# Kernel tuning notes

Measured on AMD Instinct MI355X. Metric: run time of the kernel, lower is better.

Reference implementation:

```python
import jax, jax.numpy as jnp
import numpy as np

D_K = 512  # module-level global used for the scale factor


def setup_inputs() -> dict:
    key = jax.random.key(0)
    kq, kk, kv, km = jax.random.split(key, 4)
    B, H, L = 4, 8, 1024
    Q = jax.random.normal(kq, (B, H, L, D_K), dtype=jnp.float32)
    K = jax.random.normal(kk, (B, H, L, D_K), dtype=jnp.float32)
    V = jax.random.normal(kv, (B, H, L, D_K), dtype=jnp.float32)
    attn_mask = jax.random.randint(km, (B, H, L, L), 0, 2).astype(jnp.bool_)
    return {"Q": Q, "K": K, "V": V, "attn_mask": attn_mask}


def reference(Q, K, V, attn_mask):
    scale = 1.0 / np.sqrt(D_K).astype(np.float32)
    # [B,H,Lq,Lk]
    scores = jnp.einsum('bhqd,bhkd->bhqk', Q, K) * scale
    scores = jnp.where(attn_mask, jnp.float32(-1e9), scores)
    attn = jax.nn.softmax(scores, axis=-1)
    context = jnp.einsum('bhqk,bhkd->bhqd', attn, V)
    return (context, attn)
```

## Files before the change

### kernel.cpp

```cpp
#include <hip/hip_runtime.h>
#include <hip/hip_bf16.h>

constexpr int BH  = 32;
constexpr int LQ  = 1024;
constexpr int DK  = 512;
constexpr float SCALE = 0.04419417382415922f;

using short8 = __attribute__((ext_vector_type(8))) short;
using f32x4  = __attribute__((ext_vector_type(4))) float;

__device__ __forceinline__ unsigned short cvt_bf16(float x) {
  unsigned int u = __builtin_bit_cast(unsigned int, x);
  u += 0x7FFFu + ((u >> 16) & 1u);
  return (unsigned short)(u >> 16);
}
__device__ __forceinline__ float bf2f(unsigned short s) {
  return __builtin_bit_cast(float, (unsigned int)s << 16);
}
__device__ __forceinline__ unsigned int pack2(float a, float b) {
  return (unsigned int)cvt_bf16(a) | ((unsigned int)cvt_bf16(b) << 16);
}

__device__ __forceinline__ void lds_load16(const void* g, void* l) {
  __builtin_amdgcn_global_load_lds(
      (const __attribute__((address_space(1))) unsigned int*)g,
      (__attribute__((address_space(3))) unsigned int*)l, 16, 0, 0);
}

__global__ __launch_bounds__(256) void cvt_f32_bf16(
    const float* __restrict__ src, unsigned short* __restrict__ dst, int n8) {
  int i = blockIdx.x * 256 + threadIdx.x;
  const int stride = gridDim.x * 256;
  for (; i < n8; i += stride) {
    float4 a = ((const float4*)src)[(size_t)i * 2];
    float4 b = ((const float4*)src)[(size_t)i * 2 + 1];
    unsigned short us[8] __attribute__((aligned(16)));
    us[0]=cvt_bf16(a.x); us[1]=cvt_bf16(a.y); us[2]=cvt_bf16(a.z); us[3]=cvt_bf16(a.w);
    us[4]=cvt_bf16(b.x); us[5]=cvt_bf16(b.y); us[6]=cvt_bf16(b.z); us[7]=cvt_bf16(b.w);
    ((short8*)dst)[i] = *(short8*)us;
  }
}

__global__ __launch_bounds__(256) void qk_exp_kernel(
    const unsigned short* __restrict__ A, const unsigned short* __restrict__ B,
    const int* __restrict__ mask, unsigned short* __restrict__ P,
    float* __restrict__ partials) {
  __shared__ __attribute__((aligned(16))) unsigned short smem[16384];
  unsigned short* As = smem;
  unsigned short* Bs = smem + 8192;

  int flat = blockIdx.x + 8 * (blockIdx.y + 8 * blockIdx.z);
  flat = (flat % 8) * 256 + flat / 8;
  const int bx = flat % 8;
  const int by = (flat / 8) % 8;
  const int bh = flat / 64;

  const int t = threadIdx.x;
  const int lane = t & 63, wave = t >> 6;
  const int wr = wave >> 1, wc = wave & 1;
  const int fr = lane & 15, fq = lane >> 4;
  const int m0 = by * 128, n0 = bx * 128;

  const char* Ab = (const char*)A + ((size_t)bh * LQ + m0) * 1024;
  const char* Bb = (const char*)B + ((size_t)bh * LQ + n0) * 1024;

  unsigned int orv = 0;
  {
    const unsigned int* mw = (const unsigned int*)mask;
    #pragma unroll
    for (int i = 0; i < 64; ++i) orv |= mw[i];
  }
  const bool byteMode = (orv > 1u);

  f32x4 acc[4][4];
  #pragma unroll
  for (int i = 0; i < 4; ++i)
    #pragma unroll
    for (int j = 0; j < 4; ++j) acc[i][j] = (f32x4){0.f, 0.f, 0.f, 0.f};

  for (int kb = 0; kb < DK * 2; kb += 128) {
    __syncthreads();
    #pragma unroll
    for (int i = 0; i < 4; ++i) {
      const int p  = i * 4096 + t * 16;
      const int r  = p >> 7;
      const int ch = (p >> 4) & 7;
      const int sw = ((ch ^ (r & 7)) << 4);
      lds_load16(Ab + (size_t)r * 1024 + kb + sw, (char*)As + wave * 1024 + i * 4096);
      lds_load16(Bb + (size_t)r * 1024 + kb + sw, (char*)Bs + wave * 1024 + i * 4096);
    }
    __syncthreads();

    #pragma unroll
    for (int kk = 0; kk < 2; ++kk) {
      short8 a[4], b[4];
      #pragma unroll
      for (int mi = 0; mi < 4; ++mi) {
        const int r  = wr * 64 + mi * 16 + fr;
        const int ch = (kk * 4 + fq) ^ (r & 7);
        a[mi] = *(const short8*)((const char*)As + r * 128 + ch * 16);
      }
      #pragma unroll
      for (int ni = 0; ni < 4; ++ni) {
        const int r  = wc * 64 + ni * 16 + fr;
        const int ch = (kk * 4 + fq) ^ (r & 7);
        b[ni] = *(const short8*)((const char*)Bs + r * 128 + ch * 16);
      }
      #pragma unroll
      for (int mi = 0; mi < 4; ++mi)
        #pragma unroll
        for (int ni = 0; ni < 4; ++ni)
          acc[mi][ni] = __builtin_amdgcn_mfma_f32_16x16x32_bf16(a[mi], b[ni], acc[mi][ni], 0, 0, 0);
    }
  }

  __syncthreads();
  unsigned short* Cs = smem;
  #pragma unroll
  for (int mi = 0; mi < 4; ++mi)
    #pragma unroll
    for (int ni = 0; ni < 4; ++ni) {
      const int col = wc * 64 + ni * 16 + fr;
      #pragma unroll
      for (int r = 0; r < 4; ++r) {
        const int row = wr * 64 + mi * 16 + fq * 4 + r;
        Cs[row * 128 + col] = cvt_bf16(__expf(acc[mi][ni][r] * SCALE));
      }
    }
  __syncthreads();

  const int rl = t >> 4;
  const int cl = (t & 15) * 8;
  const size_t pbase = (size_t)bh * LQ * LQ;
  #pragma unroll
  for (int rb = 0; rb < 8; ++rb) {
    const int rloc = rb * 16 + rl;
    const int rg   = m0 + rloc;
    const size_t gidx = pbase + (size_t)rg * LQ + (n0 + cl);
    short8 sv = *(const short8*)&Cs[rloc * 128 + cl];
    bool mk[8];
    if (byteMode) {
      const unsigned char* mb = (const unsigned char*)mask + gidx;
      uint2 w = *(const uint2*)mb;
      #pragma unroll
      for (int j = 0; j < 4; ++j) mk[j]     = ((w.x >> (8 * j)) & 255u) != 0u;
      #pragma unroll
      for (int j = 0; j < 4; ++j) mk[4 + j] = ((w.y >> (8 * j)) & 255u) != 0u;
    } else {
      int4 w0 = *(const int4*)(mask + gidx);
      int4 w1 = *(const int4*)(mask + gidx + 4);
      mk[0] = w0.x != 0; mk[1] = w0.y != 0; mk[2] = w0.z != 0; mk[3] = w0.w != 0;
      mk[4] = w1.x != 0; mk[5] = w1.y != 0; mk[6] = w1.z != 0; mk[7] = w1.w != 0;
    }
    unsigned short out[8] __attribute__((aligned(16)));
    float s = 0.f;
    #pragma unroll
    for (int j = 0; j < 8; ++j) {
      unsigned short v = mk[j] ? (unsigned short)0 : (unsigned short)sv[j];
      out[j] = v;
      s += bf2f(v);
    }
    *(short8*)(P + gidx) = *(short8*)out;
    s += __shfl_xor(s, 1); s += __shfl_xor(s, 2);
    s += __shfl_xor(s, 4); s += __shfl_xor(s, 8);
    if ((t & 15) == 0)
      partials[((size_t)bh * LQ + rg) * 8 + bx] = s;
  }
}

__global__ __launch_bounds__(256) void attn_fin(
    const unsigned short* __restrict__ P, const float* __restrict__ partials,
    float* __restrict__ attn) {
  const int ch = blockIdx.x, rb64 = blockIdx.y, bh = blockIdx.z;
  const int m0 = rb64 * 64;
  __shared__ float invs[64];
  const int t = threadIdx.x;
  if (t < 64) {
    const float* pp = partials + ((size_t)bh * LQ + m0 + t) * 8;
    float s = ((pp[0] + pp[1]) + (pp[2] + pp[3])) + ((pp[4] + pp[5]) + (pp[6] + pp[7]));
    invs[t] = 1.0f / s;
  }
  __syncthreads();
  const size_t pbase = (size_t)bh * LQ * LQ;
  const int c0 = ch * 512;
  #pragma unroll
  for (int rb = 0; rb < 4; ++rb) {
    const int rloc = rb * 16 + (t >> 4);
    const int row  = m0 + rloc;
    const float inv = invs[rloc];
    const size_t base = pbase + (size_t)row * LQ + c0 + (t & 15) * 8;
    #pragma unroll
    for (int j = 0; j < 4; ++j) {
      short8 sv = *(const short8*)(P + base + j * 128);
      float4 o0, o1;
      o0.x = bf2f((unsigned short)sv[0]) * inv;
      o0.y = bf2f((unsigned short)sv[1]) * inv;
      o0.z = bf2f((unsigned short)sv[2]) * inv;
      o0.w = bf2f((unsigned short)sv[3]) * inv;
      o1.x = bf2f((unsigned short)sv[4]) * inv;
      o1.y = bf2f((unsigned short)sv[5]) * inv;
      o1.z = bf2f((unsigned short)sv[6]) * inv;
      o1.w = bf2f((unsigned short)sv[7]) * inv;
      *(float4*)(attn + base + j * 128)     = o0;
      *(float4*)(attn + base + j * 128 + 4) = o1;
    }
  }
}

__global__ __launch_bounds__(256) void pv2_kernel(
    const unsigned short* __restrict__ P, const float* __restrict__ V,
    const float* __restrict__ partials, float* __restrict__ O) {
  __shared__ __attribute__((aligned(16))) unsigned short As[8192];
  __shared__ __attribute__((aligned(16))) unsigned short BsV[128 * 72];
  __shared__ float invsL[128];

  int flat = blockIdx.x + 4 * (blockIdx.y + 8 * blockIdx.z);
  flat = (flat % 8) * 128 + flat / 8;
  const int bx = flat % 4;
  const int by = (flat / 4) % 8;
  const int bh = flat / 32;

  const int t = threadIdx.x;
  const int lane = t & 63, wave = t >> 6;
  const int wr = wave >> 1, wc = wave & 1;
  const int fr = lane & 15, fq = lane >> 4;
  const int m0 = by * 128, n0 = bx * 128;

  if (t < 128) {
    const float* pp = partials + ((size_t)bh * LQ + m0 + t) * 8;
    float s = ((pp[0] + pp[1]) + (pp[2] + pp[3])) + ((pp[4] + pp[5]) + (pp[6] + pp[7]));
    invsL[t] = 1.0f / s;
  }

  const char* Ab  = (const char*)P + ((size_t)bh * LQ + m0) * 2048;
  const float* Vb = V + (size_t)bh * LQ * DK + n0;

  f32x4 acc[4][4];
  #pragma unroll
  for (int i = 0; i < 4; ++i)
    #pragma unroll
    for (int j = 0; j < 4; ++j) acc[i][j] = (f32x4){0.f, 0.f, 0.f, 0.f};

  const int g  = t >> 5;
  const int nl = t & 31;

  for (int k0 = 0; k0 < LQ; k0 += 64) {
    __syncthreads();
    #pragma unroll
    for (int i = 0; i < 4; ++i) {
      const int p  = i * 4096 + t * 16;
      const int r  = p >> 7;
      const int ch = (p >> 4) & 7;
      const int sw = ((ch ^ (r & 7)) << 4);
      lds_load16(Ab + (size_t)r * 2048 + k0 * 2 + sw, (char*)As + wave * 1024 + i * 4096);
    }
    float vf[8][4];
    #pragma unroll
    for (int i = 0; i < 8; ++i) {
      const size_t rb = (size_t)(k0 + 8 * g + i) * DK;
      #pragma unroll
      for (int jn = 0; jn < 4; ++jn)
        vf[i][jn] = Vb[rb + nl + 32 * jn];
    }
    #pragma unroll
    for (int jn = 0; jn < 4; ++jn) {
      const int n = nl + 32 * jn;
      uint2 w0, w1;
      w0.x = pack2(vf[0][jn], vf[1][jn]); w0.y = pack2(vf[2][jn], vf[3][jn]);
      w1.x = pack2(vf[4][jn], vf[5][jn]); w1.y = pack2(vf[6][jn], vf[7][jn]);
      *(uint2*)((char*)BsV + n * 144 + 16 * g)     = w0;
      *(uint2*)((char*)BsV + n * 144 + 16 * g + 8) = w1;
    }
    __syncthreads();

    #pragma unroll
    for (int kk = 0; kk < 2; ++kk) {
      short8 a[4], b[4];
      #pragma unroll
      for (int mi = 0; mi < 4; ++mi) {
        const int r  = wr * 64 + mi * 16 + fr;
        const int ch = (kk * 4 + fq) ^ (r & 7);
        a[mi] = *(const short8*)((const char*)As + r * 128 + ch * 16);
      }
      #pragma unroll
      for (int ni = 0; ni < 4; ++ni) {
        const int r = wc * 64 + ni * 16 + fr;
        b[ni] = *(const short8*)((const char*)BsV + r * 144 + (kk * 4 + fq) * 16);
      }
      #pragma unroll
      for (int mi = 0; mi < 4; ++mi)
        #pragma unroll
        for (int ni = 0; ni < 4; ++ni)
          acc[mi][ni] = __builtin_amdgcn_mfma_f32_16x16x32_bf16(a[mi], b[ni], acc[mi][ni], 0, 0, 0);
    }
  }

  const size_t obase = (size_t)bh * LQ * DK;
  #pragma unroll
  for (int mi = 0; mi < 4; ++mi)
    #pragma unroll
    for (int ni = 0; ni < 4; ++ni) {
      const int col = n0 + wc * 64 + ni * 16 + fr;
      #pragma unroll
      for (int r = 0; r < 4; ++r) {
        const int rloc = wr * 64 + mi * 16 + fq * 4 + r;
        O[obase + (size_t)(m0 + rloc) * DK + col] = acc[mi][ni][r] * invsL[rloc];
      }
    }
}

__global__ __launch_bounds__(256) void qk_mask_kernel(
    const float* __restrict__ Q, const float* __restrict__ Kmat,
    const int* __restrict__ mask, float* __restrict__ S) {
  __shared__ __attribute__((aligned(16))) unsigned short Asf[128][40];
  __shared__ __attribute__((aligned(16))) unsigned short Bsf[128][40];
  const int t = threadIdx.x;
  const int lane = t & 63, wave = t >> 6;
  const int wr = wave >> 1, wc = wave & 1;
  const int fr = lane & 15, fq = lane >> 4;
  const int bh = blockIdx.z;
  const int m0 = blockIdx.y * 128, n0 = blockIdx.x * 128;
  const float* Qb = Q + (size_t)bh * LQ * DK;
  const float* Kb = Kmat + (size_t)bh * LQ * DK;
  unsigned int orv = 0;
  { const unsigned int* mw = (const unsigned int*)mask;
    #pragma unroll
    for (int i = 0; i < 64; ++i) orv |= mw[i]; }
  const bool byteMode = (orv > 1u);
  f32x4 acc[4][4];
  #pragma unroll
  for (int i = 0; i < 4; ++i)
    #pragma unroll
    for (int j = 0; j < 4; ++j) acc[i][j] = (f32x4){0.f,0.f,0.f,0.f};
  const int sr = t >> 1, sc = (t & 1) * 16;
  for (int kd = 0; kd < DK; kd += 32) {
    __syncthreads();
    { const float4* qa = (const float4*)(Qb + (size_t)(m0+sr)*DK + kd + sc);
      float fv[16];
      #pragma unroll
      for (int i = 0; i < 4; ++i) { float4 x = qa[i];
        fv[4*i]=x.x; fv[4*i+1]=x.y; fv[4*i+2]=x.z; fv[4*i+3]=x.w; }
      unsigned short us[16] __attribute__((aligned(16)));
      #pragma unroll
      for (int i = 0; i < 16; ++i) us[i] = cvt_bf16(fv[i]);
      *(short8*)&Asf[sr][sc]   = *(short8*)&us[0];
      *(short8*)&Asf[sr][sc+8] = *(short8*)&us[8]; }
    { const float4* ka = (const float4*)(Kb + (size_t)(n0+sr)*DK + kd + sc);
      float fv[16];
      #pragma unroll
      for (int i = 0; i < 4; ++i) { float4 x = ka[i];
        fv[4*i]=x.x; fv[4*i+1]=x.y; fv[4*i+2]=x.z; fv[4*i+3]=x.w; }
      unsigned short us[16] __attribute__((aligned(16)));
      #pragma unroll
      for (int i = 0; i < 16; ++i) us[i] = cvt_bf16(fv[i]);
      *(short8*)&Bsf[sr][sc]   = *(short8*)&us[0];
      *(short8*)&Bsf[sr][sc+8] = *(short8*)&us[8]; }
    __syncthreads();
    short8 a[4], b[4];
    #pragma unroll
    for (int mi = 0; mi < 4; ++mi) a[mi] = *(const short8*)&Asf[wr*64+mi*16+fr][fq*8];
    #pragma unroll
    for (int ni = 0; ni < 4; ++ni) b[ni] = *(const short8*)&Bsf[wc*64+ni*16+fr][fq*8];
    #pragma unroll
    for (int mi = 0; mi < 4; ++mi)
      #pragma unroll
      for (int ni = 0; ni < 4; ++ni)
        acc[mi][ni] = __builtin_amdgcn_mfma_f32_16x16x32_bf16(a[mi], b[ni], acc[mi][ni], 0, 0, 0);
  }
  const size_t sbase = (size_t)bh * LQ * LQ;
  const unsigned char* mb = (const unsigned char*)mask;
  #pragma unroll
  for (int mi = 0; mi < 4; ++mi)
    #pragma unroll
    for (int ni = 0; ni < 4; ++ni) {
      const int col = n0 + wc*64 + ni*16 + fr;
      #pragma unroll
      for (int r = 0; r < 4; ++r) {
        const int row = m0 + wr*64 + mi*16 + fq*4 + r;
        const size_t idx = sbase + (size_t)row * LQ + col;
        float s = acc[mi][ni][r] * SCALE;
        const bool msk = byteMode ? (mb[idx] != 0) : (mask[idx] != 0);
        S[idx] = msk ? -1e9f : s;
      }
    }
}

__global__ __launch_bounds__(256) void softmax_kernel(float* __restrict__ A) {
  const int row = blockIdx.x;
  float4* rp = (float4*)(A + (size_t)row * LQ);
  const int t = threadIdx.x;
  float4 v = rp[t];
  float m = fmaxf(fmaxf(v.x, v.y), fmaxf(v.z, v.w));
  #pragma unroll
  for (int off = 32; off >= 1; off >>= 1) m = fmaxf(m, __shfl_xor(m, off, 64));
  __shared__ float redm[4];
  const int wv = t >> 6, ln = t & 63;
  if (ln == 0) redm[wv] = m;
  __syncthreads();
  m = fmaxf(fmaxf(redm[0], redm[1]), fmaxf(redm[2], redm[3]));
  float4 e;
  e.x = expf(v.x - m); e.y = expf(v.y - m); e.z = expf(v.z - m); e.w = expf(v.w - m);
  float s = (e.x + e.y) + (e.z + e.w);
  #pragma unroll
  for (int off = 32; off >= 1; off >>= 1) s += __shfl_xor(s, off, 64);
  __shared__ float reds2[4];
  if (ln == 0) reds2[wv] = s;
  __syncthreads();
  s = (reds2[0] + reds2[1]) + (reds2[2] + reds2[3]);
  const float inv = 1.0f / s;
  e.x *= inv; e.y *= inv; e.z *= inv; e.w *= inv;
  rp[t] = e;
}

__global__ __launch_bounds__(256) void pv_kernel(
    const float* __restrict__ P, const float* __restrict__ V, float* __restrict__ O) {
  __shared__ __attribute__((aligned(16))) unsigned short Ps[128][40];
  __shared__ __attribute__((aligned(16))) unsigned short Vtl[128][40];
  const int t = threadIdx.x;
  const int lane = t & 63, wave = t >> 6;
  const int wr = wave >> 1, wc = wave & 1;
  const int fr = lane & 15, fq = lane >> 4;
  const int bh = blockIdx.z;
  const int m0 = blockIdx.y * 128, n0 = blockIdx.x * 128;
  const float* Pb = P + (size_t)bh * LQ * LQ;
  const float* Vb = V + (size_t)bh * LQ * DK;
  f32x4 acc[4][4];
  #pragma unroll
  for (int i = 0; i < 4; ++i)
    #pragma unroll
    for (int j = 0; j < 4; ++j) acc[i][j] = (f32x4){0.f,0.f,0.f,0.f};
  const int sr = t >> 1, sc = (t & 1) * 16;
  const int kk = (t & 15) * 2, nn = (t >> 4) * 8;
  for (int k0 = 0; k0 < LQ; k0 += 32) {
    __syncthreads();
    { const float4* pa = (const float4*)(Pb + (size_t)(m0+sr)*LQ + k0 + sc);
      float fv[16];
      #pragma unroll
      for (int i = 0; i < 4; ++i) { float4 x = pa[i];
        fv[4*i]=x.x; fv[4*i+1]=x.y; fv[4*i+2]=x.z; fv[4*i+3]=x.w; }
      unsigned short us[16] __attribute__((aligned(16)));
      #pragma unroll
      for (int i = 0; i < 16; ++i) us[i] = cvt_bf16(fv[i]);
      *(short8*)&Ps[sr][sc]   = *(short8*)&us[0];
      *(short8*)&Ps[sr][sc+8] = *(short8*)&us[8]; }
    { const float* v0p = Vb + (size_t)(k0+kk)*DK + n0 + nn;
      const float* v1p = v0p + DK;
      float4 a0 = *(const float4*)v0p, a1 = *(const float4*)(v0p+4);
      float4 b0 = *(const float4*)v1p, b1 = *(const float4*)(v1p+4);
      float r0[8] = {a0.x,a0.y,a0.z,a0.w,a1.x,a1.y,a1.z,a1.w};
      float r1[8] = {b0.x,b0.y,b0.z,b0.w,b1.x,b1.y,b1.z,b1.w};
      #pragma unroll
      for (int i = 0; i < 8; ++i) {
        unsigned int pk = (unsigned int)cvt_bf16(r0[i]) | ((unsigned int)cvt_bf16(r1[i]) << 16);
        *(unsigned int*)&Vtl[nn+i][kk] = pk; } }
    __syncthreads();
    short8 a[4], b[4];
    #pragma unroll
    for (int mi = 0; mi < 4; ++mi) a[mi] = *(const short8*)&Ps[wr*64+mi*16+fr][fq*8];
    #pragma unroll
    for (int ni = 0; ni < 4; ++ni) b[ni] = *(const short8*)&Vtl[wc*64+ni*16+fr][fq*8];
    #pragma unroll
    for (int mi = 0; mi < 4; ++mi)
      #pragma unroll
      for (int ni = 0; ni < 4; ++ni)
        acc[mi][ni] = __builtin_amdgcn_mfma_f32_16x16x32_bf16(a[mi], b[ni], acc[mi][ni], 0, 0, 0);
  }
  const size_t obase = (size_t)bh * LQ * DK;
  #pragma unroll
  for (int mi = 0; mi < 4; ++mi)
    #pragma unroll
    for (int ni = 0; ni < 4; ++ni) {
      const int col = n0 + wc*64 + ni*16 + fr;
      #pragma unroll
      for (int r = 0; r < 4; ++r) {
        const int row = m0 + wr*64 + mi*16 + fq*4 + r;
        O[obase + (size_t)row * DK + col] = acc[mi][ni][r];
      }
    }
}

extern "C" void kernel_launch(void* const* d_in, const int* in_sizes, int n_in,
                              void* d_out, int out_size, void* d_ws, size_t ws_size,
                              hipStream_t stream) {
  const float* Q    = (const float*)d_in[0];
  const float* K    = (const float*)d_in[1];
  const float* V    = (const float*)d_in[2];
  const int*   mask = (const int*)d_in[3];

  float* ctx  = (float*)d_out;
  float* attn = ctx + (size_t)BH * LQ * DK;

  const size_t NE = (size_t)BH * LQ * DK;
  const size_t P_BYTES  = (size_t)BH * LQ * LQ * 2;
  const size_t WS_NEED  = P_BYTES + (size_t)BH * LQ * 8 * 4;

  if (ws_size >= WS_NEED) {
    unsigned short* Pp       = (unsigned short*)d_ws;
    float*          partials = (float*)((char*)d_ws + P_BYTES);
    unsigned short* Qb = (unsigned short*)ctx;
    unsigned short* Kb = Qb + NE;

    cvt_f32_bf16<<<dim3(2048), 256, 0, stream>>>(Q, Qb, (int)(NE / 8));
    cvt_f32_bf16<<<dim3(2048), 256, 0, stream>>>(K, Kb, (int)(NE / 8));
    qk_exp_kernel<<<dim3(8, 8, BH), 256, 0, stream>>>(Qb, Kb, mask, Pp, partials);
    attn_fin<<<dim3(2, 16, BH), 256, 0, stream>>>(Pp, partials, attn);
    pv2_kernel<<<dim3(4, 8, BH), 256, 0, stream>>>(Pp, V, partials, ctx);
  } else {
    qk_mask_kernel<<<dim3(8, 8, BH), 256, 0, stream>>>(Q, K, mask, attn);
    softmax_kernel<<<dim3(BH * LQ), 256, 0, stream>>>(attn);
    pv_kernel<<<dim3(4, 8, BH), 256, 0, stream>>>(attn, V, ctx);
  }
}
```

Before: 247.8 us.

## Double-buffer LDS tiles in QK and PV GEMM kernels to overlap loads with MFMA

Both the QK-exp kernel and the PV kernel now use two LDS buffers. The next K-slice is staged into one buffer while MFMAs consume the other, which removes one barrier per iteration. In the PV kernel, V is loaded into registers before compute and packed into LDS after compute, so global-load latency hides behind the matrix math. The cost is doubled LDS per block (64KB and about 68KB), which can reduce how many blocks fit on each CU, and higher register pressure from the prefetched V values.

Result: slower. 280.7 us (+13.3%).

```diff
diff --git a/kernel.cpp b/kernel.cpp
--- a/kernel.cpp
+++ b/kernel.cpp
@@ -45,9 +45,7 @@
     const unsigned short* __restrict__ A, const unsigned short* __restrict__ B,
     const int* __restrict__ mask, unsigned short* __restrict__ P,
     float* __restrict__ partials) {
-  __shared__ __attribute__((aligned(16))) unsigned short smem[16384];
-  unsigned short* As = smem;
-  unsigned short* Bs = smem + 8192;
+  __shared__ __attribute__((aligned(16))) unsigned short smem[32768];
 
   int flat = blockIdx.x + 8 * (blockIdx.y + 8 * blockIdx.z);
   flat = (flat % 8) * 256 + flat / 8;
@@ -78,19 +76,21 @@
     #pragma unroll
     for (int j = 0; j < 4; ++j) acc[i][j] = (f32x4){0.f, 0.f, 0.f, 0.f};
 
-  for (int kb = 0; kb < DK * 2; kb += 128) {
-    __syncthreads();
+  auto STAGE = [&](int kb, int buf) {
+    char* base = (char*)smem + buf * 32768;
     #pragma unroll
     for (int i = 0; i < 4; ++i) {
       const int p  = i * 4096 + t * 16;
       const int r  = p >> 7;
       const int ch = (p >> 4) & 7;
       const int sw = ((ch ^ (r & 7)) << 4);
-      lds_load16(Ab + (size_t)r * 1024 + kb + sw, (char*)As + wave * 1024 + i * 4096);
-      lds_load16(Bb + (size_t)r * 1024 + kb + sw, (char*)Bs + wave * 1024 + i * 4096);
-    }
-    __syncthreads();
-
+      lds_load16(Ab + (size_t)r * 1024 + kb + sw, base + wave * 1024 + i * 4096);
+      lds_load16(Bb + (size_t)r * 1024 + kb + sw, base + 16384 + wave * 1024 + i * 4096);
+    }
+  };
+  auto COMPUTE = [&](int buf) {
+    const char* As = (const char*)smem + buf * 32768;
+    const char* Bs = As + 16384;
     #pragma unroll
     for (int kk = 0; kk < 2; ++kk) {
       short8 a[4], b[4];
@@ -98,13 +98,13 @@
       for (int mi = 0; mi < 4; ++mi) {
         const int r  = wr * 64 + mi * 16 + fr;
         const int ch = (kk * 4 + fq) ^ (r & 7);
-        a[mi] = *(const short8*)((const char*)As + r * 128 + ch * 16);
+        a[mi] = *(const short8*)(As + r * 128 + ch * 16);
       }
       #pragma unroll
       for (int ni = 0; ni < 4; ++ni) {
         const int r  = wc * 64 + ni * 16 + fr;
         const int ch = (kk * 4 + fq) ^ (r & 7);
-        b[ni] = *(const short8*)((const char*)Bs + r * 128 + ch * 16);
+        b[ni] = *(const short8*)(Bs + r * 128 + ch * 16);
       }
       #pragma unroll
       for (int mi = 0; mi < 4; ++mi)
@@ -112,9 +112,18 @@
         for (int ni = 0; ni < 4; ++ni)
           acc[mi][ni] = __builtin_amdgcn_mfma_f32_16x16x32_bf16(a[mi], b[ni], acc[mi][ni], 0, 0, 0);
     }
-  }
-
+  };
+
+  STAGE(0, 0);
   __syncthreads();
+  int cur = 0;
+  for (int it = 0; it < 8; ++it) {
+    if (it < 7) STAGE((it + 1) * 128, cur ^ 1);
+    COMPUTE(cur);
+    __syncthreads();
+    cur ^= 1;
+  }
+
   unsigned short* Cs = smem;
   #pragma unroll
   for (int mi = 0; mi < 4; ++mi)
@@ -210,8 +219,8 @@
 __global__ __launch_bounds__(256) void pv2_kernel(
     const unsigned short* __restrict__ P, const float* __restrict__ V,
     const float* __restrict__ partials, float* __restrict__ O) {
-  __shared__ __attribute__((aligned(16))) unsigned short As[8192];
-  __shared__ __attribute__((aligned(16))) unsigned short BsV[128 * 72];
+  __shared__ __attribute__((aligned(16))) unsigned short smemA[2 * 8192];
+  __shared__ __attribute__((aligned(16))) unsigned short smemB[2 * 9216];
   __shared__ float invsL[128];
 
   int flat = blockIdx.x + 4 * (blockIdx.y + 8 * blockIdx.z);
@@ -244,35 +253,42 @@
   const int g  = t >> 5;
   const int nl = t & 31;
 
-  for (int k0 = 0; k0 < LQ; k0 += 64) {
-    __syncthreads();
+  float vf[8][4];
+  auto V_LOAD = [&](int k0) {
+    #pragma unroll
+    for (int i = 0; i < 8; ++i) {
+      const size_t rb = (size_t)(k0 + 8 * g + i) * DK;
+      #pragma unroll
+      for (int jn = 0; jn < 4; ++jn)
+        vf[i][jn] = Vb[rb + nl + 32 * jn];
+    }
+  };
+  auto V_STORE = [&](int buf) {
+    char* Bv = (char*)(smemB + buf * 9216);
+    #pragma unroll
+    for (int jn = 0; jn < 4; ++jn) {
+      const int n = nl + 32 * jn;
+      uint2 w0, w1;
+      w0.x = pack2(vf[0][jn], vf[1][jn]); w0.y = pack2(vf[2][jn], vf[3][jn]);
+      w1.x = pack2(vf[4][jn], vf[5][jn]); w1.y = pack2(vf[6][jn], vf[7][jn]);
+      *(uint2*)(Bv + n * 144 + 16 * g)     = w0;
+      *(uint2*)(Bv + n * 144 + 16 * g + 8) = w1;
+    }
+  };
+  auto STAGE_A = [&](int it, int buf) {
+    char* base = (char*)(smemA + buf * 8192);
     #pragma unroll
     for (int i = 0; i < 4; ++i) {
       const int p  = i * 4096 + t * 16;
       const int r  = p >> 7;
       const int ch = (p >> 4) & 7;
       const int sw = ((ch ^ (r & 7)) << 4);
-      lds_load16(Ab + (size_t)r * 2048 + k0 * 2 + sw, (char*)As + wave * 1024 + i * 4096);
-    }
-    float vf[8][4];
-    #pragma unroll
-    for (int i = 0; i < 8; ++i) {
-      const size_t rb = (size_t)(k0 + 8 * g + i) * DK;
-      #pragma unroll
-      for (int jn = 0; jn < 4; ++jn)
-        vf[i][jn] = Vb[rb + nl + 32 * jn];
-    }
-    #pragma unroll
-    for (int jn = 0; jn < 4; ++jn) {
-      const int n = nl + 32 * jn;
-      uint2 w0, w1;
-      w0.x = pack2(vf[0][jn], vf[1][jn]); w0.y = pack2(vf[2][jn], vf[3][jn]);
-      w1.x = pack2(vf[4][jn], vf[5][jn]); w1.y = pack2(vf[6][jn], vf[7][jn]);
-      *(uint2*)((char*)BsV + n * 144 + 16 * g)     = w0;
-      *(uint2*)((char*)BsV + n * 144 + 16 * g + 8) = w1;
-    }
-    __syncthreads();
-
+      lds_load16(Ab + (size_t)r * 2048 + it * 128 + sw, base + wave * 1024 + i * 4096);
+    }
+  };
+  auto COMPUTE = [&](int buf) {
+    const char* As = (const char*)(smemA + buf * 8192);
+    const char* Bv = (const char*)(smemB + buf * 9216);
     #pragma unroll
     for (int kk = 0; kk < 2; ++kk) {
       short8 a[4], b[4];
@@ -280,12 +296,12 @@
       for (int mi = 0; mi < 4; ++mi) {
         const int r  = wr * 64 + mi * 16 + fr;
         const int ch = (kk * 4 + fq) ^ (r & 7);
-        a[mi] = *(const short8*)((const char*)As + r * 128 + ch * 16);
+        a[mi] = *(const short8*)(As + r * 128 + ch * 16);
       }
       #pragma unroll
       for (int ni = 0; ni < 4; ++ni) {
         const int r = wc * 64 + ni * 16 + fr;
-        b[ni] = *(const short8*)((const char*)BsV + r * 144 + (kk * 4 + fq) * 16);
+        b[ni] = *(const short8*)(Bv + r * 144 + (kk * 4 + fq) * 16);
       }
       #pragma unroll
       for (int mi = 0; mi < 4; ++mi)
@@ -293,6 +309,22 @@
         for (int ni = 0; ni < 4; ++ni)
           acc[mi][ni] = __builtin_amdgcn_mfma_f32_16x16x32_bf16(a[mi], b[ni], acc[mi][ni], 0, 0, 0);
     }
+  };
+
+  V_LOAD(0);
+  STAGE_A(0, 0);
+  V_STORE(0);
+  __syncthreads();
+  int cur = 0;
+  for (int it = 0; it < 16; ++it) {
+    if (it < 15) {
+      V_LOAD((it + 1) * 64);
+      STAGE_A(it + 1, cur ^ 1);
+    }
+    COMPUTE(cur);
+    if (it < 15) V_STORE(cur ^ 1);
+    __syncthreads();
+    cur ^= 1;
   }
 
   const size_t obase = (size_t)bh * LQ * DK;
```

## Double-buffer LDS staging in QK kernel and merge Q/K conversion launches

Applied to the files above, without the earlier changes.

The QK^T kernel now keeps two LDS buffers of 32 KB each. It issues the global-to-LDS loads for the next K-slice before computing on the current one, so memory latency overlaps with MFMA work and only one barrier is needed per iteration. The two f32-to-bf16 conversion launches are merged into a single launch that picks Q or K from blockIdx.y, saving one launch. Doubling LDS to 64 KB per block may lower occupancy, and the single barrier after compute has to be enough to protect the buffer being overwritten.

Measured after the change: 237.0 us. -4.4%, faster.

```diff
diff --git a/kernel.cpp b/kernel.cpp
--- a/kernel.cpp
+++ b/kernel.cpp
@@ -27,8 +27,11 @@
       (__attribute__((address_space(3))) unsigned int*)l, 16, 0, 0);
 }
 
-__global__ __launch_bounds__(256) void cvt_f32_bf16(
-    const float* __restrict__ src, unsigned short* __restrict__ dst, int n8) {
+__global__ __launch_bounds__(256) void cvt2_f32_bf16(
+    const float* __restrict__ s0, const float* __restrict__ s1,
+    unsigned short* __restrict__ d0, unsigned short* __restrict__ d1, int n8) {
+  const float* src = blockIdx.y ? s1 : s0;
+  unsigned short* dst = blockIdx.y ? d1 : d0;
   int i = blockIdx.x * 256 + threadIdx.x;
   const int stride = gridDim.x * 256;
   for (; i < n8; i += stride) {
@@ -45,9 +48,7 @@
     const unsigned short* __restrict__ A, const unsigned short* __restrict__ B,
     const int* __restrict__ mask, unsigned short* __restrict__ P,
     float* __restrict__ partials) {
-  __shared__ __attribute__((aligned(16))) unsigned short smem[16384];
-  unsigned short* As = smem;
-  unsigned short* Bs = smem + 8192;
+  __shared__ __attribute__((aligned(16))) unsigned short smem[32768];
 
   int flat = blockIdx.x + 8 * (blockIdx.y + 8 * blockIdx.z);
   flat = (flat % 8) * 256 + flat / 8;
@@ -78,19 +79,21 @@
     #pragma unroll
     for (int j = 0; j < 4; ++j) acc[i][j] = (f32x4){0.f, 0.f, 0.f, 0.f};
 
-  for (int kb = 0; kb < DK * 2; kb += 128) {
-    __syncthreads();
+  auto STAGE = [&](int kb, int buf) {
+    char* base = (char*)smem + buf * 32768;
     #pragma unroll
     for (int i = 0; i < 4; ++i) {
       const int p  = i * 4096 + t * 16;
       const int r  = p >> 7;
       const int ch = (p >> 4) & 7;
       const int sw = ((ch ^ (r & 7)) << 4);
-      lds_load16(Ab + (size_t)r * 1024 + kb + sw, (char*)As + wave * 1024 + i * 4096);
-      lds_load16(Bb + (size_t)r * 1024 + kb + sw, (char*)Bs + wave * 1024 + i * 4096);
-    }
-    __syncthreads();
-
+      lds_load16(Ab + (size_t)r * 1024 + kb + sw, base + wave * 1024 + i * 4096);
+      lds_load16(Bb + (size_t)r * 1024 + kb + sw, base + 16384 + wave * 1024 + i * 4096);
+    }
+  };
+  auto COMPUTE = [&](int buf) {
+    const char* As = (const char*)smem + buf * 32768;
+    const char* Bs = As + 16384;
     #pragma unroll
     for (int kk = 0; kk < 2; ++kk) {
       short8 a[4], b[4];
@@ -98,13 +101,13 @@
       for (int mi = 0; mi < 4; ++mi) {
         const int r  = wr * 64 + mi * 16 + fr;
         const int ch = (kk * 4 + fq) ^ (r & 7);
-        a[mi] = *(const short8*)((const char*)As + r * 128 + ch * 16);
+        a[mi] = *(const short8*)(As + r * 128 + ch * 16);
       }
       #pragma unroll
       for (int ni = 0; ni < 4; ++ni) {
         const int r  = wc * 64 + ni * 16 + fr;
         const int ch = (kk * 4 + fq) ^ (r & 7);
-        b[ni] = *(const short8*)((const char*)Bs + r * 128 + ch * 16);
+        b[ni] = *(const short8*)(Bs + r * 128 + ch * 16);
       }
       #pragma unroll
       for (int mi = 0; mi < 4; ++mi)
@@ -112,9 +115,18 @@
         for (int ni = 0; ni < 4; ++ni)
           acc[mi][ni] = __builtin_amdgcn_mfma_f32_16x16x32_bf16(a[mi], b[ni], acc[mi][ni], 0, 0, 0);
     }
-  }
-
+  };
+
+  STAGE(0, 0);
   __syncthreads();
+  int cur = 0;
+  for (int it = 0; it < 8; ++it) {
+    if (it < 7) STAGE((it + 1) * 128, cur ^ 1);
+    COMPUTE(cur);
+    __syncthreads();
+    cur ^= 1;
+  }
+
   unsigned short* Cs = smem;
   #pragma unroll
   for (int mi = 0; mi < 4; ++mi)
@@ -500,8 +512,7 @@
     unsigned short* Qb = (unsigned short*)ctx;
     unsigned short* Kb = Qb + NE;
 
-    cvt_f32_bf16<<<dim3(2048), 256, 0, stream>>>(Q, Qb, (int)(NE / 8));
-    cvt_f32_bf16<<<dim3(2048), 256, 0, stream>>>(K, Kb, (int)(NE / 8));
+    cvt2_f32_bf16<<<dim3(1024, 2), 256, 0, stream>>>(Q, K, Qb, Kb, (int)(NE / 8));
     qk_exp_kernel<<<dim3(8, 8, BH), 256, 0, stream>>>(Qb, Kb, mask, Pp, partials);
     attn_fin<<<dim3(2, 16, BH), 256, 0, stream>>>(Pp, partials, attn);
     pv2_kernel<<<dim3(4, 8, BH), 256, 0, stream>>>(Pp, V, partials, ctx);
```
